# Kernel tuning notes

Measured on AMD Instinct MI355X. Metric: run time of the kernel, lower is better.

The kernel has to match this reference:

```python
import jax, jax.numpy as jnp
import numpy as np

B, S, D, H, L, FF, V, T = 4, 160, 512, 8, 2, 2048, 50000, 256
Wd = D // H


def layer_norm(x, g, b, eps=1e-12):
    u = x.mean(-1, keepdims=True)
    s = ((x - u) ** 2).mean(-1, keepdims=True)
    return g * (x - u) / jnp.sqrt(s + eps) + b


def setup_inputs() -> dict:
    key = jax.random.key(0)
    ks = jax.random.split(key, 16)
    sc = 0.02
    inp = {
        'x': jax.random.randint(ks[0], (B, S), 0, V),
        'stamp': jax.random.randint(ks[1], (B, S - 1, 3), 0, 8),
        'mask': jnp.ones((B, S), dtype=jnp.int32),
        'time_matrix': jax.random.randint(ks[2], (B, S, S), 0, T + 1),
        'tok_emb': jax.random.normal(ks[3], (V, D)) * sc,
        'month_emb': jax.random.normal(ks[4], (13, D)) * sc,
        'day_emb': jax.random.normal(ks[5], (32, D)) * sc,
        'tiK_emb': jax.random.normal(ks[6], (T + 1, D)) * sc,
        'tiV_emb': jax.random.normal(ks[7], (T + 1, D)) * sc,
        'g0': jnp.ones((D,)), 'b0': jnp.zeros((D,)),
        'Wq': jax.random.normal(ks[8], (L, D, D)) * sc, 'bq': jnp.zeros((L, D)),
        'Wk': jax.random.normal(ks[9], (L, D, D)) * sc, 'bk': jnp.zeros((L, D)),
        'Wv': jax.random.normal(ks[10], (L, D, D)) * sc, 'bv': jnp.zeros((L, D)),
        'Wo': jax.random.normal(ks[11], (L, D, D)) * sc, 'bo': jnp.zeros((L, D)),
        'g1': jnp.ones((L, D)), 'b1': jnp.zeros((L, D)),
        'W1': jax.random.normal(ks[12], (L, D, FF)) * sc, 'c1': jnp.zeros((L, FF)),
        'W2': jax.random.normal(ks[13], (L, FF, D)) * sc, 'c2': jnp.zeros((L, D)),
        'g2': jnp.ones((L, D)), 'b2': jnp.zeros((L, D)),
    }
    return inp


def reference(x, stamp, mask, time_matrix, tok_emb, month_emb, day_emb,
              tiK_emb, tiV_emb, g0, b0, Wq, bq, Wk, bk, Wv, bv, Wo, bo,
              g1, b1, W1, c1, W2, c2, g2, b2):
    # Embeddings: month + day temporal embed, one zero timestep prepended
    t_e = month_emb[stamp[..., 0]] + day_emb[stamp[..., 1]]          # [B,S-1,D]
    t_e = jnp.concatenate([jnp.zeros((B, 1, D), t_e.dtype), t_e], axis=1)
    h = layer_norm(tok_emb[x] + t_e, g0, b0)                         # [B,S,D]
    tK = tiK_emb[time_matrix].reshape(B, S, S, H, Wd)                # [B,S,S,H,W]
    tV = tiV_emb[time_matrix].reshape(B, S, S, H, Wd)
    maskf = mask.astype(h.dtype)
    # faithful to original: +10000*(1-mask), added AFTER scaling
    bias = 10000.0 * (1.0 - maskf)[:, None, None, :]
    inv_sqrt = 1.0 / jnp.sqrt(jnp.asarray(Wd, h.dtype))
    for l in range(L):
        q = (h @ Wq[l] + bq[l]).reshape(B, S, H, Wd).transpose(0, 2, 1, 3)  # [B,H,S,W]
        k = (h @ Wk[l] + bk[l]).reshape(B, S, H, Wd).transpose(0, 2, 1, 3)
        v = (h @ Wv[l] + bv[l]).reshape(B, S, H, Wd).transpose(0, 2, 1, 3)
        scores = (jnp.einsum('bhiw,bhjw->bhij', q, k)
                  + jnp.einsum('bijhw,bhiw->bhij', tK, q)) * inv_sqrt + bias
        attn = jax.nn.softmax(scores, axis=-1)                        # [B,H,S,S]
        # standard value mix + diagonal of attn-weighted t_V (relative-time values)
        hh = (jnp.einsum('bhij,bhjw->bihw', attn, v)
              + jnp.einsum('bhik,bikhw->bihw', attn, tV)).reshape(B, S, D)
        h = layer_norm(h + hh @ Wo[l] + bo[l], g1[l], b1[l])
        ff = jax.nn.gelu(h @ W1[l] + c1[l], approximate=False) @ W2[l] + c2[l]
        h = layer_norm(h + ff, g2[l], b2[l])
    return h
```

## Files before the change

kernel.cpp:

```cpp
#include <hip/hip_runtime.h>
#include <hip/hip_bf16.h>
#include <math.h>

#define SS 160
#define DD 512
#define HH 8
#define MTOK 640
#define FFD 2048
#define NTT 257

typedef __attribute__((ext_vector_type(8))) short bfrag8;
typedef __attribute__((ext_vector_type(4))) float facc4;
typedef unsigned short u16;

#define SWZ(row, cb) ((cb) ^ (((row)&7) << 4))

__device__ __forceinline__ void gload16(const void* g, void* l) {
  __builtin_amdgcn_global_load_lds(
      (const __attribute__((address_space(1))) void*)g,
      (__attribute__((address_space(3))) void*)l, 16, 0, 0);
}

__device__ void wconv_body(const float* __restrict__ src,
                           __hip_bfloat16* __restrict__ dst,
                           int K, int N, int dls, int rowoff,
                           int l, int bx, int by, float (*tile)[65])
{
  src += (size_t)l * K * N;
  dst += (size_t)l * dls + (size_t)rowoff * K;
  int k0 = by * 64, n0 = bx * 64;
  int t = threadIdx.x;
  int r = t >> 2, c0 = (t & 3) * 16;
  #pragma unroll
  for (int j = 0; j < 16; j += 4) {
    float4 v4 = *(const float4*)&src[(size_t)(k0 + r) * N + n0 + c0 + j];
    tile[r][c0 + j + 0] = v4.x; tile[r][c0 + j + 1] = v4.y;
    tile[r][c0 + j + 2] = v4.z; tile[r][c0 + j + 3] = v4.w;
  }
  __syncthreads();
  union { u16 u[8]; uint4 v; } pk;
  #pragma unroll
  for (int half = 0; half < 2; ++half) {
    #pragma unroll
    for (int j = 0; j < 8; ++j) {
      __hip_bfloat16 hb = __float2bfloat16(tile[c0 + half * 8 + j][r]);
      pk.u[j] = *reinterpret_cast<u16*>(&hb);
    }
    *(uint4*)&dst[(size_t)(n0 + r) * K + k0 + c0 + half * 8] = pk.v;
  }
}

__global__ __launch_bounds__(256) void prep_all(
    const float* __restrict__ Wq, const float* __restrict__ Wk,
    const float* __restrict__ Wv, const float* __restrict__ Wo,
    const float* __restrict__ W1, const float* __restrict__ W2,
    const float* __restrict__ tiK,
    __hip_bfloat16* __restrict__ wqkv, __hip_bfloat16* __restrict__ wo_t,
    __hip_bfloat16* __restrict__ w1_t, __hip_bfloat16* __restrict__ w2_t,
    __hip_bfloat16* __restrict__ tikb,
    const int* __restrict__ x, const int* __restrict__ stamp,
    const float* __restrict__ tok, const float* __restrict__ month,
    const float* __restrict__ day, const float* __restrict__ g0,
    const float* __restrict__ b0, float* __restrict__ h,
    __hip_bfloat16* __restrict__ hb)
{
  __shared__ float tile[64][65];
  __shared__ float ssh[4], qsh[4];
  int idx = blockIdx.x;
  int tid = threadIdx.x;

  if (idx < 1536) {
    if (idx < 384) {
      int grp = idx / 128, r = idx % 128;
      int l = r / 64, t = r % 64;
      const float* src = grp == 0 ? Wq : (grp == 1 ? Wk : Wv);
      wconv_body(src, wqkv, 512, 512, 1536 * 512, 512 * grp, l, t % 8, t / 8, tile);
    } else if (idx < 512) {
      int r = idx - 384; int l = r / 64, t = r % 64;
      wconv_body(Wo, wo_t, 512, 512, 512 * 512, 0, l, t % 8, t / 8, tile);
    } else if (idx < 1024) {
      int r = idx - 512; int l = r / 256, t = r % 256;
      wconv_body(W1, w1_t, 512, 2048, 2048 * 512, 0, l, t % 32, t / 32, tile);
    } else {
      int r = idx - 1024; int l = r / 256, t = r % 256;
      wconv_body(W2, w2_t, 2048, 512, 512 * 2048, 0, l, t % 8, t / 8, tile);
    }
  } else if (idx < 1665) {
    int i = (idx - 1536) * 256 + tid;
    if (i < NTT * DD / 4) {
      float4 v = *(const float4*)(tiK + (size_t)i * 4);
      union { u16 u[4]; uint2 w; } pk;
      __hip_bfloat16 h0 = __float2bfloat16(v.x), h1 = __float2bfloat16(v.y);
      __hip_bfloat16 h2 = __float2bfloat16(v.z), h3 = __float2bfloat16(v.w);
      pk.u[0] = *(u16*)&h0; pk.u[1] = *(u16*)&h1;
      pk.u[2] = *(u16*)&h2; pk.u[3] = *(u16*)&h3;
      *(uint2*)(tikb + (size_t)i * 4) = pk.w;
    }
  } else {
    int m = idx - 1665;
    int b = m / SS, s = m % SS, t = tid;
    int tokid = x[m];
    float v0 = tok[tokid * DD + t];
    float v1 = tok[tokid * DD + t + 256];
    if (s > 0) {
      int sidx = (b * (SS - 1) + (s - 1)) * 3;
      int mo = stamp[sidx + 0], dy = stamp[sidx + 1];
      v0 += month[mo * DD + t]       + day[dy * DD + t];
      v1 += month[mo * DD + t + 256] + day[dy * DD + t + 256];
    }
    float sum = v0 + v1, sq = v0 * v0 + v1 * v1;
    #pragma unroll
    for (int off = 1; off < 64; off <<= 1) {
      sum += __shfl_xor(sum, off);
      sq  += __shfl_xor(sq , off);
    }
    if ((t & 63) == 0) { ssh[t >> 6] = sum; qsh[t >> 6] = sq; }
    __syncthreads();
    float fsum = ssh[0] + ssh[1] + ssh[2] + ssh[3];
    float fsq  = qsh[0] + qsh[1] + qsh[2] + qsh[3];
    float u = fsum * (1.0f / 512.0f);
    float var = fsq * (1.0f / 512.0f) - u * u;
    float r = rsqrtf(var + 1e-12f);
    float y0 = g0[t]       * ((v0 - u) * r) + b0[t];
    float y1 = g0[t + 256] * ((v1 - u) * r) + b0[t + 256];
    h[m * DD + t]        = y0;  h[m * DD + t + 256]  = y1;
    hb[m * DD + t]       = __float2bfloat16(y0);
    hb[m * DD + t + 256] = __float2bfloat16(y1);
  }
}

__global__ __launch_bounds__(256) void ln_kernel(
    const float* __restrict__ in, const float* __restrict__ g,
    const float* __restrict__ b, float* __restrict__ out,
    __hip_bfloat16* __restrict__ outb)
{
  int m = blockIdx.x; int t = threadIdx.x;
  float v0 = in[m*DD + t];
  float v1 = in[m*DD + t + 256];
  float sum = v0+v1, sq = v0*v0+v1*v1;
  #pragma unroll
  for (int off=1; off<64; off<<=1) {
    sum += __shfl_xor(sum, off);
    sq  += __shfl_xor(sq , off);
  }
  __shared__ float ssh[4], qsh[4];
  if ((t&63)==0) { ssh[t>>6]=sum; qsh[t>>6]=sq; }
  __syncthreads();
  float fsum = ssh[0]+ssh[1]+ssh[2]+ssh[3];
  float fsq  = qsh[0]+qsh[1]+qsh[2]+qsh[3];
  float u = fsum * (1.0f/512.0f);
  float var = fsq * (1.0f/512.0f) - u*u;
  float r = rsqrtf(var + 1e-12f);
  float y0 = g[t]    *((v0-u)*r) + b[t];
  float y1 = g[t+256]*((v1-u)*r) + b[t+256];
  out[m*DD+t]     = y0;
  out[m*DD+t+256] = y1;
  if (outb) {
    outb[m*DD+t]     = __float2bfloat16(y0);
    outb[m*DD+t+256] = __float2bfloat16(y1);
  }
}

#define EPI_RESID 1
#define EPI_GELU 2
#define EPI_QKV 3

template<int EPI, int K>
__global__ __launch_bounds__(256) void gemm_ck(
    const __hip_bfloat16* __restrict__ A,
    const __hip_bfloat16* __restrict__ Bt,
    const float* __restrict__ bias,
    const float* __restrict__ bias2,
    const float* __restrict__ bias3,
    const float* __restrict__ resid,
    float* __restrict__ Cf,
    __hip_bfloat16* __restrict__ Cb,
    int N)
{
  constexpr int KC = 128;
  constexpr int NCH = K / KC;
  __shared__ u16 As[2][64 * KC];
  __shared__ u16 Bs[2][64 * KC];
  const int tid = threadIdx.x, wv = tid >> 6, lane = tid & 63;
  const int m0 = blockIdx.y * 64, n0 = blockIdx.x * 64;
  const int wr = wv >> 1, wc = wv & 1;
  const int fr = lane & 15, fks = lane >> 4;

  const int ldsq = (wv * 4) * 1024;
  const int off0 = ldsq + lane * 16;

  #define STAGE(c, buf) do {                                                  \
    _Pragma("unroll")                                                         \
    for (int i_ = 0; i_ < 4; ++i_) {                                          \
      int ldso = ldsq + i_ * 1024;                                            \
      int off = off0 + i_ * 1024;                                             \
      int r_ = off >> 8;                                                      \
      int p_ = off & 255;                                                     \
      int ps_ = p_ ^ ((r_ & 7) << 4);                                         \
      gload16((const char*)A  + ((size_t)(m0 + r_) * K + (c) * KC) * 2 + ps_, \
              (char*)&As[buf][0] + ldso);                                     \
      gload16((const char*)Bt + ((size_t)(n0 + r_) * K + (c) * KC) * 2 + ps_, \
              (char*)&Bs[buf][0] + ldso);                                     \
    }                                                                         \
  } while (0)

  facc4 acc[2][2] = {};
  STAGE(0, 0);
  STAGE(1, 1);

  #pragma unroll
  for (int c = 0; c < NCH; ++c) {
    if (c + 1 < NCH) asm volatile("s_waitcnt vmcnt(8)\n\ts_barrier" ::: "memory");
    else             asm volatile("s_waitcnt vmcnt(0)\n\ts_barrier" ::: "memory");
    const char* ab = (const char*)&As[c & 1][0];
    const char* bb = (const char*)&Bs[c & 1][0];
    #pragma unroll
    for (int ks = 0; ks < 4; ++ks) {
      bfrag8 af[2], bfv[2];
      #pragma unroll
      for (int mf = 0; mf < 2; ++mf) {
        int rA = wr * 32 + mf * 16 + fr;
        af[mf] = *(const bfrag8*)(ab + rA * 256 + SWZ(rA, ks * 64 + fks * 16));
      }
      #pragma unroll
      for (int nf = 0; nf < 2; ++nf) {
        int rB = wc * 32 + nf * 16 + fr;
        bfv[nf] = *(const bfrag8*)(bb + rB * 256 + SWZ(rB, ks * 64 + fks * 16));
      }
      #pragma unroll
      for (int mf = 0; mf < 2; ++mf)
        #pragma unroll
        for (int nf = 0; nf < 2; ++nf)
          acc[mf][nf] = __builtin_amdgcn_mfma_f32_16x16x32_bf16(
              af[mf], bfv[nf], acc[mf][nf], 0, 0, 0);
    }
    asm volatile("s_barrier" ::: "memory");
    if (c + 2 < NCH) STAGE(c + 2, c & 1);
  }
  #undef STAGE

  #pragma unroll
  for (int mf = 0; mf < 2; ++mf) {
    #pragma unroll
    for (int nf = 0; nf < 2; ++nf) {
      int col = n0 + wc * 32 + nf * 16 + fr;
      float bb;
      if (EPI == EPI_QKV)
        bb = col < 512 ? bias[col] : (col < 1024 ? bias2[col - 512] : bias3[col - 1024]);
      else
        bb = bias[col];
      #pragma unroll
      for (int j = 0; j < 4; ++j) {
        int row = m0 + wr * 32 + mf * 16 + fks * 4 + j;
        float c = acc[mf][nf][j] + bb;
        if (EPI == EPI_RESID) {
          c += resid[(size_t)row * N + col];
          Cf[(size_t)row * N + col] = c;
        } else {
          if (EPI == EPI_GELU) c = 0.5f * c * (1.0f + erff(c * 0.70710678118654752f));
          Cb[(size_t)row * N + col] = __float2bfloat16(c);
        }
      }
    }
  }
}

__global__ __launch_bounds__(256) void skg_kernel(
    const __hip_bfloat16* __restrict__ qkv,
    const __hip_bfloat16* __restrict__ tikb,
    float* __restrict__ Sk, float* __restrict__ G)
{
  __shared__ u16 As[64 * 64];
  __shared__ u16 Bs[64 * 64];
  const int tid = threadIdx.x;
  const int wid = tid >> 6, lane = tid & 63;
  const int wr = wid >> 1, wc = wid & 1;
  const int fr = lane & 15, fks = lane >> 4;
  const int sr = tid >> 2, sc = (tid & 3) * 16;
  const int swz0 = sr * 128 + SWZ(sr, sc * 2);
  const int swz1 = sr * 128 + SWZ(sr, sc * 2 + 16);
  int idx = blockIdx.x;

  if (idx < 288) {
    const int z = idx / 9, rem = idx % 9;
    const int m0 = (rem / 3) * 64, n0 = (rem % 3) * 64;
    const int b = z >> 3, h = z & 7;
    const __hip_bfloat16* Aq = qkv + (size_t)b * SS * 1536 + h * 64;
    const __hip_bfloat16* Bt = qkv + (size_t)b * SS * 1536 + 512 + h * 64;
    float* C = Sk + (size_t)z * SS * SS;
    const int ar = min(m0 + sr, SS - 1), br = min(n0 + sr, SS - 1);
    uint4 av0 = *(const uint4*)(Aq + (size_t)ar * 1536 + sc);
    uint4 av1 = *(const uint4*)(Aq + (size_t)ar * 1536 + sc + 8);
    uint4 bv0 = *(const uint4*)(Bt + (size_t)br * 1536 + sc);
    uint4 bv1 = *(const uint4*)(Bt + (size_t)br * 1536 + sc + 8);
    *(uint4*)((char*)As + swz0) = av0;
    *(uint4*)((char*)As + swz1) = av1;
    *(uint4*)((char*)Bs + swz0) = bv0;
    *(uint4*)((char*)Bs + swz1) = bv1;
    __syncthreads();
    facc4 acc[2][2] = {};
    #pragma unroll
    for (int ks = 0; ks < 2; ++ks) {
      bfrag8 af[2], bfv[2];
      #pragma unroll
      for (int mf = 0; mf < 2; ++mf) {
        int rA = wr * 32 + mf * 16 + fr;
        af[mf] = *(const bfrag8*)((const char*)As + rA * 128 + SWZ(rA, 64 * ks + 16 * fks));
      }
      #pragma unroll
      for (int nf = 0; nf < 2; ++nf) {
        int rB = wc * 32 + nf * 16 + fr;
        bfv[nf] = *(const bfrag8*)((const char*)Bs + rB * 128 + SWZ(rB, 64 * ks + 16 * fks));
      }
      #pragma unroll
      for (int mf = 0; mf < 2; ++mf)
        #pragma unroll
        for (int nf = 0; nf < 2; ++nf)
          acc[mf][nf] = __builtin_amdgcn_mfma_f32_16x16x32_bf16(
              af[mf], bfv[nf], acc[mf][nf], 0, 0, 0);
    }
    #pragma unroll
    for (int mf = 0; mf < 2; ++mf)
      #pragma unroll
      for (int nf = 0; nf < 2; ++nf) {
        int col = n0 + wc * 32 + nf * 16 + fr;
        #pragma unroll
        for (int j = 0; j < 4; ++j) {
          int row = m0 + wr * 32 + mf * 16 + fks * 4 + j;
          if (row < SS && col < SS) C[row * SS + col] = acc[mf][nf][j];
        }
      }
  } else {
    int i2 = idx - 288;
    const int nb = i2 % 5, mb = (i2 / 5) % 10, h = i2 / 50;
    const int m0 = mb * 64, n0 = nb * 64;
    const __hip_bfloat16* Aq = qkv + h * 64;
    const __hip_bfloat16* Bt = tikb + h * 64;
    const int br = min(n0 + sr, NTT - 1);
    uint4 av0 = *(const uint4*)(Aq + (size_t)(m0 + sr) * 1536 + sc);
    uint4 av1 = *(const uint4*)(Aq + (size_t)(m0 + sr) * 1536 + sc + 8);
    uint4 bv0 = *(const uint4*)(Bt + (size_t)br * 512 + sc);
    uint4 bv1 = *(const uint4*)(Bt + (size_t)br * 512 + sc + 8);
    *(uint4*)((char*)As + swz0) = av0;
    *(uint4*)((char*)As + swz1) = av1;
    *(uint4*)((char*)Bs + swz0) = bv0;
    *(uint4*)((char*)Bs + swz1) = bv1;
    __syncthreads();
    facc4 acc[2][2] = {};
    #pragma unroll
    for (int ks = 0; ks < 2; ++ks) {
      bfrag8 af[2], bfv[2];
      #pragma unroll
      for (int mf = 0; mf < 2; ++mf) {
        int rA = wr * 32 + mf * 16 + fr;
        af[mf] = *(const bfrag8*)((const char*)As + rA * 128 + SWZ(rA, 64 * ks + 16 * fks));
      }
      #pragma unroll
      for (int nf = 0; nf < 2; ++nf) {
        int rB = wc * 32 + nf * 16 + fr;
        bfv[nf] = *(const bfrag8*)((const char*)Bs + rB * 128 + SWZ(rB, 64 * ks + 16 * fks));
      }
      #pragma unroll
      for (int mf = 0; mf < 2; ++mf)
        #pragma unroll
        for (int nf = 0; nf < 2; ++nf)
          acc[mf][nf] = __builtin_amdgcn_mfma_f32_16x16x32_bf16(
              af[mf], bfv[nf], acc[mf][nf], 0, 0, 0);
    }
    #pragma unroll
    for (int mf = 0; mf < 2; ++mf)
      #pragma unroll
      for (int nf = 0; nf < 2; ++nf) {
        int col = n0 + wc * 32 + nf * 16 + fr;
        #pragma unroll
        for (int j = 0; j < 4; ++j) {
          int row = m0 + wr * 32 + mf * 16 + fks * 4 + j;
          if (col < NTT)
            G[((size_t)h * MTOK + row) * NTT + col] = acc[mf][nf][j];
        }
      }
  }
}

__global__ __launch_bounds__(256) void attn2(
    const __hip_bfloat16* __restrict__ qkv,
    const float* __restrict__ Sk, const float* __restrict__ G,
    const int* __restrict__ tm, const int* __restrict__ mask,
    const float* __restrict__ tiV, __hip_bfloat16* __restrict__ hh)
{
  const int h = blockIdx.y, b = blockIdx.z;
  const int ib0 = blockIdx.x * 8;
  const int tid = threadIdx.x, wv = tid >> 6, lane = tid & 63;
  __shared__ float P[8][176];
  __shared__ int tmsh[8][176];

  float rinvs[2];
  #pragma unroll
  for (int rr = 0; rr < 2; ++rr) {
    const int r = wv * 2 + rr, i = ib0 + r, m = b * SS + i;
    const float* Grow = G + ((size_t)h * MTOK + m) * NTT;
    const float* Srow = Sk + ((size_t)(b * 8 + h) * SS + i) * SS;
    const int* tmrow = tm + (size_t)m * SS;
    float sv[3];
    float mx = -1e30f;
    #pragma unroll
    for (int g = 0; g < 3; ++g) {
      int j = lane + g * 64;
      if (j < SS) {
        int t = tmrow[j];
        tmsh[r][j] = t;
        float s = (Srow[j] + Grow[t]) * 0.125f
                + 10000.0f * (1.0f - (float)mask[b * SS + j]);
        sv[g] = s; mx = fmaxf(mx, s);
      } else sv[g] = -1e30f;
    }
    #pragma unroll
    for (int off = 1; off < 64; off <<= 1) mx = fmaxf(mx, __shfl_xor(mx, off));
    float sum = 0.f;
    #pragma unroll
    for (int g = 0; g < 3; ++g) {
      int j = lane + g * 64;
      if (j < SS) { float p = expf(sv[g] - mx); P[r][j] = p; sum += p; }
    }
    #pragma unroll
    for (int off = 1; off < 64; off <<= 1) sum += __shfl_xor(sum, off);
    rinvs[rr] = 1.0f / sum;
  }

  const int r0 = wv * 2, r1 = r0 + 1;
  const int i0 = ib0 + r0, i1 = ib0 + r1;
  const __hip_bfloat16* vbase = qkv + (size_t)b * SS * 1536 + 1024 + h * 64 + lane;
  const float* tvbase = tiV + h * 64 + lane;
  float acc0 = 0.f, acc1 = 0.f;
  #pragma unroll 4
  for (int j = 0; j < SS; ++j) {
    float vv = __bfloat162float(vbase[(size_t)j * 1536]);
    float a0 = P[r0][j], a1 = P[r1][j];
    int t0 = tmsh[r0][j], t1 = tmsh[r1][j];
    acc0 += a0 * (vv + tvbase[(size_t)t0 * 512]);
    acc1 += a1 * (vv + tvbase[(size_t)t1 * 512]);
  }
  hh[((size_t)(b * SS) + i0) * DD + h * 64 + lane] = __float2bfloat16(acc0 * rinvs[0]);
  hh[((size_t)(b * SS) + i1) * DD + h * 64 + lane] = __float2bfloat16(acc1 * rinvs[1]);
}

extern "C" void kernel_launch(void* const* d_in, const int* in_sizes, int n_in,
                              void* d_out, int out_size, void* d_ws, size_t ws_size,
                              hipStream_t stream) {
  const int*   x     = (const int*)d_in[0];
  const int*   stamp = (const int*)d_in[1];
  const int*   mask  = (const int*)d_in[2];
  const int*   tm    = (const int*)d_in[3];
  const float* tok   = (const float*)d_in[4];
  const float* month = (const float*)d_in[5];
  const float* day   = (const float*)d_in[6];
  const float* tiK   = (const float*)d_in[7];
  const float* tiV   = (const float*)d_in[8];
  const float* g0    = (const float*)d_in[9];
  const float* b0    = (const float*)d_in[10];
  const float* Wq    = (const float*)d_in[11];
  const float* bq    = (const float*)d_in[12];
  const float* Wk    = (const float*)d_in[13];
  const float* bk    = (const float*)d_in[14];
  const float* Wv    = (const float*)d_in[15];
  const float* bv    = (const float*)d_in[16];
  const float* Wo    = (const float*)d_in[17];
  const float* bo    = (const float*)d_in[18];
  const float* g1    = (const float*)d_in[19];
  const float* b1    = (const float*)d_in[20];
  const float* W1    = (const float*)d_in[21];
  const float* c1    = (const float*)d_in[22];
  const float* W2    = (const float*)d_in[23];
  const float* c2    = (const float*)d_in[24];
  const float* g2    = (const float*)d_in[25];
  const float* b2    = (const float*)d_in[26];

  float* out = (float*)d_out;
  const size_t NT = (size_t)MTOK * DD;

  char* p = (char*)d_ws;
  float* h    = (float*)p;  p += NT * 4;
  float* tb   = (float*)p;  p += NT * 4;
  float* Skb  = (float*)p;  p += (size_t)32 * SS * SS * 4;
  float* Gb   = (float*)p;  p += (size_t)HH * MTOK * NTT * 4;
  __hip_bfloat16* h_bf   = (__hip_bfloat16*)p;  p += NT * 2;
  __hip_bfloat16* hh_bf  = (__hip_bfloat16*)p;  p += NT * 2;
  __hip_bfloat16* fb_bf  = (__hip_bfloat16*)p;  p += (size_t)MTOK * FFD * 2;
  __hip_bfloat16* qkv_bf = (__hip_bfloat16*)p;  p += (size_t)MTOK * 1536 * 2;
  __hip_bfloat16* tikb   = (__hip_bfloat16*)p;  p += (size_t)NTT * DD * 2;
  __hip_bfloat16* wqkv   = (__hip_bfloat16*)p;  p += (size_t)2 * 1536 * 512 * 2;
  __hip_bfloat16* wo_t   = (__hip_bfloat16*)p;  p += (size_t)2 * 512 * 512 * 2;
  __hip_bfloat16* w1_t   = (__hip_bfloat16*)p;  p += (size_t)2 * 2048 * 512 * 2;
  __hip_bfloat16* w2_t   = (__hip_bfloat16*)p;  p += (size_t)2 * 512 * 2048 * 2;

  prep_all<<<2305, 256, 0, stream>>>(Wq, Wk, Wv, Wo, W1, W2, tiK,
                                     wqkv, wo_t, w1_t, w2_t, tikb,
                                     x, stamp, tok, month, day, g0, b0, h, h_bf);

  for (int l = 0; l < 2; ++l) {
    gemm_ck<EPI_QKV, 512><<<dim3(24, 10), 256, 0, stream>>>(
        h_bf, wqkv + (size_t)l * 1536 * 512, bq + l*DD, bk + l*DD, bv + l*DD,
        nullptr, nullptr, qkv_bf, 1536);

    skg_kernel<<<688, 256, 0, stream>>>(qkv_bf, tikb, Skb, Gb);

    attn2<<<dim3(20, 8, 4), 256, 0, stream>>>(qkv_bf, Skb, Gb, tm, mask, tiV, hh_bf);

    gemm_ck<EPI_RESID, 512><<<dim3(8, 10), 256, 0, stream>>>(
        hh_bf, wo_t + (size_t)l * 512 * 512, bo + l*DD, nullptr, nullptr,
        h, tb, nullptr, 512);
    ln_kernel<<<MTOK, 256, 0, stream>>>(tb, g1 + l*DD, b1 + l*DD, h, h_bf);

    gemm_ck<EPI_GELU, 512><<<dim3(32, 10), 256, 0, stream>>>(
        h_bf, w1_t + (size_t)l * 2048 * 512, c1 + l*FFD, nullptr, nullptr,
        nullptr, nullptr, fb_bf, 2048);

    gemm_ck<EPI_RESID, 2048><<<dim3(8, 10), 256, 0, stream>>>(
        fb_bf, w2_t + (size_t)l * 512 * 2048, c2 + l*DD, nullptr, nullptr,
        h, tb, nullptr, 512);
    ln_kernel<<<MTOK, 256, 0, stream>>>(tb, g2 + l*DD, b2 + l*DD,
                                        (l == 1) ? out : h,
                                        (l == 1) ? nullptr : h_bf);
  }
}
```

Baseline: 147.9 us.

## Fuse score and time-key GEMMs into attention kernel via in-block MFMA

```diff
diff --git a/kernel.cpp b/kernel.cpp
--- a/kernel.cpp
+++ b/kernel.cpp
@@ -19,6 +19,11 @@
   __builtin_amdgcn_global_load_lds(
       (const __attribute__((address_space(1))) void*)g,
       (__attribute__((address_space(3))) void*)l, 16, 0, 0);
+}
+
+__device__ __forceinline__ u16 f2b(float f) {
+  __hip_bfloat16 hb = __float2bfloat16(f);
+  return *reinterpret_cast<u16*>(&hb);
 }
 
 __device__ void wconv_body(const float* __restrict__ src,
@@ -42,10 +47,8 @@
   #pragma unroll
   for (int half = 0; half < 2; ++half) {
     #pragma unroll
-    for (int j = 0; j < 8; ++j) {
-      __hip_bfloat16 hb = __float2bfloat16(tile[c0 + half * 8 + j][r]);
-      pk.u[j] = *reinterpret_cast<u16*>(&hb);
-    }
+    for (int j = 0; j < 8; ++j)
+      pk.u[j] = f2b(tile[c0 + half * 8 + j][r]);
     *(uint4*)&dst[(size_t)(n0 + r) * K + k0 + c0 + half * 8] = pk.v;
   }
 }
@@ -90,10 +93,8 @@
     if (i < NTT * DD / 4) {
       float4 v = *(const float4*)(tiK + (size_t)i * 4);
       union { u16 u[4]; uint2 w; } pk;
-      __hip_bfloat16 h0 = __float2bfloat16(v.x), h1 = __float2bfloat16(v.y);
-      __hip_bfloat16 h2 = __float2bfloat16(v.z), h3 = __float2bfloat16(v.w);
-      pk.u[0] = *(u16*)&h0; pk.u[1] = *(u16*)&h1;
-      pk.u[2] = *(u16*)&h2; pk.u[3] = *(u16*)&h3;
+      pk.u[0] = f2b(v.x); pk.u[1] = f2b(v.y);
+      pk.u[2] = f2b(v.z); pk.u[3] = f2b(v.w);
       *(uint2*)(tikb + (size_t)i * 4) = pk.w;
     }
   } else {
@@ -265,141 +266,63 @@
   }
 }
 
-__global__ __launch_bounds__(256) void skg_kernel(
+__global__ __launch_bounds__(256) void attn_f(
     const __hip_bfloat16* __restrict__ qkv,
     const __hip_bfloat16* __restrict__ tikb,
-    float* __restrict__ Sk, float* __restrict__ G)
-{
-  __shared__ u16 As[64 * 64];
-  __shared__ u16 Bs[64 * 64];
-  const int tid = threadIdx.x;
-  const int wid = tid >> 6, lane = tid & 63;
-  const int wr = wid >> 1, wc = wid & 1;
-  const int fr = lane & 15, fks = lane >> 4;
-  const int sr = tid >> 2, sc = (tid & 3) * 16;
-  const int swz0 = sr * 128 + SWZ(sr, sc * 2);
-  const int swz1 = sr * 128 + SWZ(sr, sc * 2 + 16);
-  int idx = blockIdx.x;
-
-  if (idx < 288) {
-    const int z = idx / 9, rem = idx % 9;
-    const int m0 = (rem / 3) * 64, n0 = (rem % 3) * 64;
-    const int b = z >> 3, h = z & 7;
-    const __hip_bfloat16* Aq = qkv + (size_t)b * SS * 1536 + h * 64;
-    const __hip_bfloat16* Bt = qkv + (size_t)b * SS * 1536 + 512 + h * 64;
-    float* C = Sk + (size_t)z * SS * SS;
-    const int ar = min(m0 + sr, SS - 1), br = min(n0 + sr, SS - 1);
-    uint4 av0 = *(const uint4*)(Aq + (size_t)ar * 1536 + sc);
-    uint4 av1 = *(const uint4*)(Aq + (size_t)ar * 1536 + sc + 8);
-    uint4 bv0 = *(const uint4*)(Bt + (size_t)br * 1536 + sc);
-    uint4 bv1 = *(const uint4*)(Bt + (size_t)br * 1536 + sc + 8);
-    *(uint4*)((char*)As + swz0) = av0;
-    *(uint4*)((char*)As + swz1) = av1;
-    *(uint4*)((char*)Bs + swz0) = bv0;
-    *(uint4*)((char*)Bs + swz1) = bv1;
-    __syncthreads();
-    facc4 acc[2][2] = {};
-    #pragma unroll
-    for (int ks = 0; ks < 2; ++ks) {
-      bfrag8 af[2], bfv[2];
-      #pragma unroll
-      for (int mf = 0; mf < 2; ++mf) {
-        int rA = wr * 32 + mf * 16 + fr;
-        af[mf] = *(const bfrag8*)((const char*)As + rA * 128 + SWZ(rA, 64 * ks + 16 * fks));
-      }
-      #pragma unroll
-      for (int nf = 0; nf < 2; ++nf) {
-        int rB = wc * 32 + nf * 16 + fr;
-        bfv[nf] = *(const bfrag8*)((const char*)Bs + rB * 128 + SWZ(rB, 64 * ks + 16 * fks));
-      }
-      #pragma unroll
-      for (int mf = 0; mf < 2; ++mf)
-        #pragma unroll
-        for (int nf = 0; nf < 2; ++nf)
-          acc[mf][nf] = __builtin_amdgcn_mfma_f32_16x16x32_bf16(
-              af[mf], bfv[nf], acc[mf][nf], 0, 0, 0);
-    }
-    #pragma unroll
-    for (int mf = 0; mf < 2; ++mf)
-      #pragma unroll
-      for (int nf = 0; nf < 2; ++nf) {
-        int col = n0 + wc * 32 + nf * 16 + fr;
-        #pragma unroll
-        for (int j = 0; j < 4; ++j) {
-          int row = m0 + wr * 32 + mf * 16 + fks * 4 + j;
-          if (row < SS && col < SS) C[row * SS + col] = acc[mf][nf][j];
-        }
-      }
-  } else {
-    int i2 = idx - 288;
-    const int nb = i2 % 5, mb = (i2 / 5) % 10, h = i2 / 50;
-    const int m0 = mb * 64, n0 = nb * 64;
-    const __hip_bfloat16* Aq = qkv + h * 64;
-    const __hip_bfloat16* Bt = tikb + h * 64;
-    const int br = min(n0 + sr, NTT - 1);
-    uint4 av0 = *(const uint4*)(Aq + (size_t)(m0 + sr) * 1536 + sc);
-    uint4 av1 = *(const uint4*)(Aq + (size_t)(m0 + sr) * 1536 + sc + 8);
-    uint4 bv0 = *(const uint4*)(Bt + (size_t)br * 512 + sc);
-    uint4 bv1 = *(const uint4*)(Bt + (size_t)br * 512 + sc + 8);
-    *(uint4*)((char*)As + swz0) = av0;
-    *(uint4*)((char*)As + swz1) = av1;
-    *(uint4*)((char*)Bs + swz0) = bv0;
-    *(uint4*)((char*)Bs + swz1) = bv1;
-    __syncthreads();
-    facc4 acc[2][2] = {};
-    #pragma unroll
-    for (int ks = 0; ks < 2; ++ks) {
-      bfrag8 af[2], bfv[2];
-      #pragma unroll
-      for (int mf = 0; mf < 2; ++mf) {
-        int rA = wr * 32 + mf * 16 + fr;
-        af[mf] = *(const bfrag8*)((const char*)As + rA * 128 + SWZ(rA, 64 * ks + 16 * fks));
-      }
-      #pragma unroll
-      for (int nf = 0; nf < 2; ++nf) {
-        int rB = wc * 32 + nf * 16 + fr;
-        bfv[nf] = *(const bfrag8*)((const char*)Bs + rB * 128 + SWZ(rB, 64 * ks + 16 * fks));
-      }
-      #pragma unroll
-      for (int mf = 0; mf < 2; ++mf)
-        #pragma unroll
-        for (int nf = 0; nf < 2; ++nf)
-          acc[mf][nf] = __builtin_amdgcn_mfma_f32_16x16x32_bf16(
-              af[mf], bfv[nf], acc[mf][nf], 0, 0, 0);
-    }
-    #pragma unroll
-    for (int mf = 0; mf < 2; ++mf)
-      #pragma unroll
-      for (int nf = 0; nf < 2; ++nf) {
-        int col = n0 + wc * 32 + nf * 16 + fr;
-        #pragma unroll
-        for (int j = 0; j < 4; ++j) {
-          int row = m0 + wr * 32 + mf * 16 + fks * 4 + j;
-          if (col < NTT)
-            G[((size_t)h * MTOK + row) * NTT + col] = acc[mf][nf][j];
-        }
-      }
-  }
-}
-
-__global__ __launch_bounds__(256) void attn2(
-    const __hip_bfloat16* __restrict__ qkv,
-    const float* __restrict__ Sk, const float* __restrict__ G,
     const int* __restrict__ tm, const int* __restrict__ mask,
     const float* __restrict__ tiV, __hip_bfloat16* __restrict__ hh)
 {
   const int h = blockIdx.y, b = blockIdx.z;
-  const int ib0 = blockIdx.x * 8;
+  const int i0 = blockIdx.x * 8;
   const int tid = threadIdx.x, wv = tid >> 6, lane = tid & 63;
+  const int fr = lane & 15, fks = lane >> 4;
+  __shared__ float S[8][160];
+  __shared__ float Gsh[8][272];
   __shared__ float P[8][176];
   __shared__ int tmsh[8][176];
 
+  bfrag8 aq0, aq1;
+  {
+    const __hip_bfloat16* qrow =
+        qkv + (size_t)(b * SS + i0 + (fr < 8 ? fr : 7)) * 1536 + h * 64;
+    aq0 = *(const bfrag8*)(qrow + fks * 8);
+    aq1 = *(const bfrag8*)(qrow + 32 + fks * 8);
+  }
+  for (int tt = wv; tt < 27; tt += 4) {
+    facc4 acc = {};
+    if (tt < 10) {
+      int j = tt * 16 + fr;
+      const __hip_bfloat16* krow = qkv + (size_t)(b * SS + j) * 1536 + 512 + h * 64;
+      bfrag8 b0 = *(const bfrag8*)(krow + fks * 8);
+      bfrag8 b1 = *(const bfrag8*)(krow + 32 + fks * 8);
+      acc = __builtin_amdgcn_mfma_f32_16x16x32_bf16(aq0, b0, acc, 0, 0, 0);
+      acc = __builtin_amdgcn_mfma_f32_16x16x32_bf16(aq1, b1, acc, 0, 0, 0);
+      #pragma unroll
+      for (int jj = 0; jj < 4; ++jj) {
+        int qr = fks * 4 + jj;
+        if (qr < 8) S[qr][tt * 16 + fr] = acc[jj];
+      }
+    } else {
+      int t0 = (tt - 10) * 16;
+      int t = min(t0 + fr, NTT - 1);
+      const __hip_bfloat16* trow = tikb + (size_t)t * 512 + h * 64;
+      bfrag8 b0 = *(const bfrag8*)(trow + fks * 8);
+      bfrag8 b1 = *(const bfrag8*)(trow + 32 + fks * 8);
+      acc = __builtin_amdgcn_mfma_f32_16x16x32_bf16(aq0, b0, acc, 0, 0, 0);
+      acc = __builtin_amdgcn_mfma_f32_16x16x32_bf16(aq1, b1, acc, 0, 0, 0);
+      #pragma unroll
+      for (int jj = 0; jj < 4; ++jj) {
+        int qr = fks * 4 + jj;
+        if (qr < 8) Gsh[qr][t0 + fr] = acc[jj];
+      }
+    }
+  }
+  __syncthreads();
+
   float rinvs[2];
   #pragma unroll
   for (int rr = 0; rr < 2; ++rr) {
-    const int r = wv * 2 + rr, i = ib0 + r, m = b * SS + i;
-    const float* Grow = G + ((size_t)h * MTOK + m) * NTT;
-    const float* Srow = Sk + ((size_t)(b * 8 + h) * SS + i) * SS;
+    const int r = wv * 2 + rr, i = i0 + r, m = b * SS + i;
     const int* tmrow = tm + (size_t)m * SS;
     float sv[3];
     float mx = -1e30f;
@@ -409,7 +332,7 @@
       if (j < SS) {
         int t = tmrow[j];
         tmsh[r][j] = t;
-        float s = (Srow[j] + Grow[t]) * 0.125f
+        float s = (S[r][j] + Gsh[r][t]) * 0.125f
                 + 10000.0f * (1.0f - (float)mask[b * SS + j]);
         sv[g] = s; mx = fmaxf(mx, s);
       } else sv[g] = -1e30f;
@@ -428,7 +351,7 @@
   }
 
   const int r0 = wv * 2, r1 = r0 + 1;
-  const int i0 = ib0 + r0, i1 = ib0 + r1;
+  const int ii0 = i0 + r0, ii1 = i0 + r1;
   const __hip_bfloat16* vbase = qkv + (size_t)b * SS * 1536 + 1024 + h * 64 + lane;
   const float* tvbase = tiV + h * 64 + lane;
   float acc0 = 0.f, acc1 = 0.f;
@@ -440,8 +363,8 @@
     acc0 += a0 * (vv + tvbase[(size_t)t0 * 512]);
     acc1 += a1 * (vv + tvbase[(size_t)t1 * 512]);
   }
-  hh[((size_t)(b * SS) + i0) * DD + h * 64 + lane] = __float2bfloat16(acc0 * rinvs[0]);
-  hh[((size_t)(b * SS) + i1) * DD + h * 64 + lane] = __float2bfloat16(acc1 * rinvs[1]);
+  hh[((size_t)(b * SS) + ii0) * DD + h * 64 + lane] = __float2bfloat16(acc0 * rinvs[0]);
+  hh[((size_t)(b * SS) + ii1) * DD + h * 64 + lane] = __float2bfloat16(acc1 * rinvs[1]);
 }
 
 extern "C" void kernel_launch(void* const* d_in, const int* in_sizes, int n_in,
@@ -481,8 +404,6 @@
   char* p = (char*)d_ws;
   float* h    = (float*)p;  p += NT * 4;
   float* tb   = (float*)p;  p += NT * 4;
-  float* Skb  = (float*)p;  p += (size_t)32 * SS * SS * 4;
-  float* Gb   = (float*)p;  p += (size_t)HH * MTOK * NTT * 4;
   __hip_bfloat16* h_bf   = (__hip_bfloat16*)p;  p += NT * 2;
   __hip_bfloat16* hh_bf  = (__hip_bfloat16*)p;  p += NT * 2;
   __hip_bfloat16* fb_bf  = (__hip_bfloat16*)p;  p += (size_t)MTOK * FFD * 2;
@@ -502,9 +423,7 @@
         h_bf, wqkv + (size_t)l * 1536 * 512, bq + l*DD, bk + l*DD, bv + l*DD,
         nullptr, nullptr, qkv_bf, 1536);
 
-    skg_kernel<<<688, 256, 0, stream>>>(qkv_bf, tikb, Skb, Gb);
-
-    attn2<<<dim3(20, 8, 4), 256, 0, stream>>>(qkv_bf, Skb, Gb, tm, mask, tiV, hh_bf);
+    attn_f<<<dim3(20, 8, 4), 256, 0, stream>>>(qkv_bf, tikb, tm, mask, tiV, hh_bf);
 
     gemm_ck<EPI_RESID, 512><<<dim3(8, 10), 256, 0, stream>>>(
         hh_bf, wo_t + (size_t)l * 512 * 512, bo + l*DD, nullptr, nullptr,
```

Result: no change. 146.3 us (-1.1%).
